# Kernel optimization log

Measured on AMD Instinct MI355X. Metric: run time of the kernel, lower is better.

The kernel has to match this reference:

```python
import jax, jax.numpy as jnp
import numpy as np

EMB = 1024
HEADS = 16
HEAD_DIM = EMB // HEADS
FF = 4 * EMB


def _gelu_tanh(x):
    c = jnp.sqrt(jnp.asarray(2.0 / jnp.pi, x.dtype))
    return 0.5 * x * (1.0 + jnp.tanh(c * (x + 0.044715 * x ** 3)))


def _layernorm(x, scale, shift, eps=1e-5):
    mean = jnp.mean(x, axis=-1, keepdims=True)
    var = jnp.mean((x - mean) ** 2, axis=-1, keepdims=True)
    return scale * (x - mean) / jnp.sqrt(var + eps) + shift


def setup_inputs() -> dict:
    key = jax.random.key(0)
    ks = jax.random.split(key, 8)
    s = 0.02
    return {
        "x": jax.random.normal(ks[0], (2, 2048, EMB), jnp.float32),
        "w_q": jax.random.normal(ks[1], (EMB, EMB), jnp.float32) * s,
        "w_k": jax.random.normal(ks[2], (EMB, EMB), jnp.float32) * s,
        "w_v": jax.random.normal(ks[3], (EMB, EMB), jnp.float32) * s,
        "w_o": jax.random.normal(ks[4], (EMB, EMB), jnp.float32) * s,
        "b_o": jnp.zeros((EMB,), jnp.float32),
        "ln1_scale": jnp.ones((EMB,), jnp.float32),
        "ln1_shift": jnp.zeros((EMB,), jnp.float32),
        "ln2_scale": jnp.ones((EMB,), jnp.float32),
        "ln2_shift": jnp.zeros((EMB,), jnp.float32),
        "w_ff1": jax.random.normal(ks[5], (EMB, FF), jnp.float32) * s,
        "b_ff1": jnp.zeros((FF,), jnp.float32),
        "w_ff2": jax.random.normal(ks[6], (FF, EMB), jnp.float32) * s,
        "b_ff2": jnp.zeros((EMB,), jnp.float32),
    }


def _attention(x, w_q, w_k, w_v, w_o, b_o):
    b, n, _ = x.shape
    q = (x @ w_q).reshape(b, n, HEADS, HEAD_DIM).transpose(0, 2, 1, 3)  # bhnd
    k = (x @ w_k).reshape(b, n, HEADS, HEAD_DIM).transpose(0, 2, 1, 3)
    v = (x @ w_v).reshape(b, n, HEADS, HEAD_DIM).transpose(0, 2, 1, 3)
    scores = jnp.einsum("bhqd,bhkd->bhqk", q, k)
    causal = jnp.triu(jnp.ones((n, n), bool), k=1)
    scores = jnp.where(causal, -jnp.inf, scores)
    # original scales AFTER masking (-inf stays -inf)
    attn = jax.nn.softmax(scores / jnp.sqrt(jnp.asarray(HEAD_DIM, x.dtype)), axis=-1)
    ctx = jnp.einsum("bhqk,bhkd->bhqd", attn, v)
    ctx = ctx.transpose(0, 2, 1, 3).reshape(b, n, EMB)
    return ctx @ w_o + b_o


def reference(x, w_q, w_k, w_v, w_o, b_o, ln1_scale, ln1_shift,
              ln2_scale, ln2_shift, w_ff1, b_ff1, w_ff2, b_ff2):
    h = _layernorm(x, ln1_scale, ln1_shift)
    h = _attention(h, w_q, w_k, w_v, w_o, b_o)
    x = x + h  # dropout is identity at drop_rate=0 / eval
    h = _layernorm(x, ln2_scale, ln2_shift)
    h = _gelu_tanh(h @ w_ff1 + b_ff1) @ w_ff2 + b_ff2
    return x + h
```

## Files before the change

### kernel.cpp

```cpp
#include <hip/hip_runtime.h>
#include <math.h>

#define EMB 1024
#define HEADS 16
#define HD 64
#define FF_DIM 4096
#define SEQ 2048
#define BATCH 2
#define NTOK (BATCH * SEQ)

typedef __bf16 bf16x8 __attribute__((ext_vector_type(8)));
typedef float f32x4 __attribute__((ext_vector_type(4)));

__device__ __forceinline__ unsigned short f2bf(float f) {
    union { float f; unsigned int u; } v; v.f = f;
    unsigned int r = v.u + 0x7fff + ((v.u >> 16) & 1);
    return (unsigned short)(r >> 16);
}

__device__ __forceinline__ unsigned int cvt_pk_bf16(float a, float b) {
    unsigned int r;
    asm("v_cvt_pk_bf16_f32 %0, %1, %2" : "=v"(r) : "v"(a), "v"(b));
    return r;
}

__device__ __forceinline__ float gelu_f(float x) {
    const float A = 1.5957691216057308f;
    const float B = 0.07135481282989427f;
    float zz = x * (A + B * x * x);
    return x * __builtin_amdgcn_rcpf(1.f + __expf(-zz));
}

#define GLOAD_LDS16(g, l)                                                      \
    __builtin_amdgcn_global_load_lds(                                          \
        (const __attribute__((address_space(1))) void*)(g),                    \
        (__attribute__((address_space(3))) void*)(l), 16, 0, 0)

__global__ __launch_bounds__(256) void ln_kernel(const float* __restrict__ x,
                                                 const float* __restrict__ scale,
                                                 const float* __restrict__ shift,
                                                 unsigned short* __restrict__ out) {
    int row = blockIdx.x;
    const float4* xr = (const float4*)(x + (size_t)row * EMB);
    int t = threadIdx.x;

    float4 v = xr[t];
    float s = v.x + v.y + v.z + v.w;
    float s2 = v.x * v.x + v.y * v.y + v.z * v.z + v.w * v.w;
    for (int o = 32; o > 0; o >>= 1) {
        s += __shfl_down(s, o, 64);
        s2 += __shfl_down(s2, o, 64);
    }
    __shared__ float red[4], red2[4];
    int wave = t >> 6;
    if ((t & 63) == 0) { red[wave] = s; red2[wave] = s2; }
    __syncthreads();
    if (t == 0) {
        float a = 0.f, b = 0.f;
#pragma unroll
        for (int i = 0; i < 4; i++) { a += red[i]; b += red2[i]; }
        red[0] = a; red2[0] = b;
    }
    __syncthreads();
    float mean = red[0] * (1.f / EMB);
    float var = red2[0] * (1.f / EMB) - mean * mean;
    float rstd = rsqrtf(var + 1e-5f);

    float4 sc = ((const float4*)scale)[t];
    float4 sh = ((const float4*)shift)[t];
    ushort4 o;
    o.x = f2bf(sc.x * (v.x - mean) * rstd + sh.x);
    o.y = f2bf(sc.y * (v.y - mean) * rstd + sh.y);
    o.z = f2bf(sc.z * (v.z - mean) * rstd + sh.z);
    o.w = f2bf(sc.w * (v.w - mean) * rstd + sh.w);
    ((ushort4*)(out + (size_t)row * EMB))[t] = o;
}

__global__ __launch_bounds__(256) void prep_kernel(
    const float* __restrict__ w0, const float* __restrict__ w1,
    const float* __restrict__ w2, const float* __restrict__ w3,
    const float* __restrict__ w4, const float* __restrict__ w5,
    unsigned short* __restrict__ o0, unsigned short* __restrict__ o1,
    unsigned short* __restrict__ o2, unsigned short* __restrict__ o3,
    unsigned short* __restrict__ o4, unsigned short* __restrict__ o5,
    const float* __restrict__ x, const float* __restrict__ ln1s,
    const float* __restrict__ ln1b, unsigned short* __restrict__ lnO) {
    __shared__ float tile[64][65];
    __shared__ float red[4], red2[4];
    int id = blockIdx.x;
    int t = threadIdx.x;

    if (id >= 3072) {
        int row = id - 3072;
        const float4* xr = (const float4*)(x + (size_t)row * EMB);
        float4 v = xr[t];
        float s = v.x + v.y + v.z + v.w;
        float s2 = v.x * v.x + v.y * v.y + v.z * v.z + v.w * v.w;
        for (int o = 32; o > 0; o >>= 1) {
            s += __shfl_down(s, o, 64);
            s2 += __shfl_down(s2, o, 64);
        }
        int wave = t >> 6;
        if ((t & 63) == 0) { red[wave] = s; red2[wave] = s2; }
        __syncthreads();
        if (t == 0) {
            float a = 0.f, b = 0.f;
#pragma unroll
            for (int i = 0; i < 4; i++) { a += red[i]; b += red2[i]; }
            red[0] = a; red2[0] = b;
        }
        __syncthreads();
        float mean = red[0] * (1.f / EMB);
        float var = red2[0] * (1.f / EMB) - mean * mean;
        float rstd = rsqrtf(var + 1e-5f);

        float4 sc = ((const float4*)ln1s)[t];
        float4 sh = ((const float4*)ln1b)[t];
        ushort4 o;
        o.x = f2bf(sc.x * (v.x - mean) * rstd + sh.x);
        o.y = f2bf(sc.y * (v.y - mean) * rstd + sh.y);
        o.z = f2bf(sc.z * (v.z - mean) * rstd + sh.z);
        o.w = f2bf(sc.w * (v.w - mean) * rstd + sh.w);
        ((ushort4*)(lnO + (size_t)row * EMB))[t] = o;
        return;
    }

    const float* src; unsigned short* dst; int K, N, lid;
    if (id < 256)       { src = w0; dst = o0; K = 1024; N = 1024; lid = id; }
    else if (id < 512)  { src = w1; dst = o1; K = 1024; N = 1024; lid = id - 256; }
    else if (id < 768)  { src = w2; dst = o2; K = 1024; N = 1024; lid = id - 512; }
    else if (id < 1024) { src = w3; dst = o3; K = 1024; N = 1024; lid = id - 768; }
    else if (id < 2048) { src = w4; dst = o4; K = 1024; N = 4096; lid = id - 1024; }
    else                { src = w5; dst = o5; K = 4096; N = 1024; lid = id - 2048; }
    int tn = N >> 6;
    int k0 = (lid / tn) << 6, n0 = (lid % tn) << 6;
    int rr = t >> 6, cc = t & 63;
#pragma unroll
    for (int i = 0; i < 16; i++) {
        int r = i * 4 + rr;
        tile[r][cc] = src[(size_t)(k0 + r) * N + n0 + cc];
    }
    __syncthreads();
#pragma unroll
    for (int i = 0; i < 16; i++) {
        int r = i * 4 + rr;
        dst[(size_t)(n0 + r) * K + k0 + cc] = f2bf(tile[cc][r]);
    }
}


__global__ __launch_bounds__(256) void ff1_gemm(
    const unsigned short* __restrict__ A,
    const unsigned short* __restrict__ Bt,
    unsigned short* __restrict__ C,
    const float* __restrict__ bias,
    int M, int N, int K) {
    __shared__ unsigned short As[2][128 * 64];
    __shared__ unsigned short Bs[2][128 * 64];

    const int t = threadIdx.x;
    const int w = t >> 6, lane = t & 63;
    const int m0 = blockIdx.x * 128, n0 = blockIdx.y * 128;

    const int srow = lane >> 3;
    const int sc = (lane & 7) ^ srow;
    const unsigned short* gA[4];
    const unsigned short* gB[4];
#pragma unroll
    for (int i = 0; i < 4; i++) {
        gA[i] = A + (size_t)(m0 + i * 32 + w * 8 + srow) * K + sc * 8;
        gB[i] = Bt + (size_t)(n0 + i * 32 + w * 8 + srow) * K + sc * 8;
    }

    const int mrow = (w >> 1) * 64, ncol = (w & 1) * 64;
    int ph[2];
#pragma unroll
    for (int s = 0; s < 2; s++) ph[s] = ((s * 4 + (lane >> 4)) ^ (lane & 7)) * 8;
    int abase[4], bbase[4];
#pragma unroll
    for (int i = 0; i < 4; i++) {
        abase[i] = (mrow + i * 16 + (lane & 15)) * 64;
        bbase[i] = (ncol + i * 16 + (lane & 15)) * 64;
    }

    f32x4 acc[4][4];
#pragma unroll
    for (int i = 0; i < 4; i++)
#pragma unroll
        for (int j = 0; j < 4; j++) acc[i][j] = (f32x4){0.f, 0.f, 0.f, 0.f};

#define STG1(b)                                                                \
    do {                                                                       \
        _Pragma("unroll") for (int i_ = 0; i_ < 4; i_++) {                     \
            GLOAD_LDS16(gA[i_], &As[b][(i_ * 32 + w * 8) * 64]);               \
            GLOAD_LDS16(gB[i_], &Bs[b][(i_ * 32 + w * 8) * 64]);               \
            gA[i_] += 64; gB[i_] += 64;                                        \
        }                                                                      \
    } while (0)

    STG1(0);
    const int nk = K >> 6;
    for (int it = 0; it < nk; it++) {
        const int buf = it & 1;
        __syncthreads();
        if (it + 1 < nk) STG1(buf ^ 1);
#pragma unroll
        for (int s = 0; s < 2; s++) {
            bf16x8 af[4], bfr[4];
#pragma unroll
            for (int i = 0; i < 4; i++) {
                af[i] = *reinterpret_cast<const bf16x8*>(&As[buf][abase[i] + ph[s]]);
                bfr[i] = *reinterpret_cast<const bf16x8*>(&Bs[buf][bbase[i] + ph[s]]);
            }
#pragma unroll
            for (int i = 0; i < 4; i++)
#pragma unroll
                for (int j = 0; j < 4; j++)
                    acc[i][j] = __builtin_amdgcn_mfma_f32_16x16x32_bf16(
                        af[i], bfr[j], acc[i][j], 0, 0, 0);
        }
    }
#undef STG1

    const int ccol = lane & 15;
    const int crow = (lane >> 4) << 2;
#pragma unroll
    for (int i = 0; i < 4; i++) {
#pragma unroll
        for (int j = 0; j < 4; j++) {
            int col = n0 + ncol + j * 16 + ccol;
            float badd = bias[col];
#pragma unroll
            for (int r = 0; r < 4; r++) {
                int row = m0 + mrow + i * 16 + crow + r;
                C[(size_t)row * N + col] = f2bf(gelu_f(acc[i][j][r] + badd));
            }
        }
    }
}

template <int EPI>
__global__ __launch_bounds__(256) void mfma_gemm_s64(
    const unsigned short* __restrict__ A,
    const unsigned short* __restrict__ Bt,
    float* __restrict__ C,
    const float* __restrict__ bias,
    const float* __restrict__ resid,
    int M, int N, int K) {
    __shared__ unsigned short As[2][64 * 64];
    __shared__ unsigned short Bs[2][64 * 64];

    const int t = threadIdx.x;
    const int w = t >> 6, lane = t & 63;
    const int m0 = blockIdx.x * 64, n0 = blockIdx.y * 64;

    const int srow = lane >> 3;
    const int sc = (lane & 7) ^ srow;
    const unsigned short* gA[2];
    const unsigned short* gB[2];
#pragma unroll
    for (int i = 0; i < 2; i++) {
        gA[i] = A + (size_t)(m0 + i * 32 + w * 8 + srow) * K + sc * 8;
        gB[i] = Bt + (size_t)(n0 + i * 32 + w * 8 + srow) * K + sc * 8;
    }

    int ph[2];
#pragma unroll
    for (int s = 0; s < 2; s++) ph[s] = ((s * 4 + (lane >> 4)) ^ (lane & 7)) * 8;
    const int mrow = (w >> 1) * 32, ncol = (w & 1) * 32;
    int abase[2], bbase[2];
#pragma unroll
    for (int i = 0; i < 2; i++) {
        abase[i] = (mrow + i * 16 + (lane & 15)) * 64;
        bbase[i] = (ncol + i * 16 + (lane & 15)) * 64;
    }

    f32x4 acc[2][2];
#pragma unroll
    for (int i = 0; i < 2; i++)
#pragma unroll
        for (int j = 0; j < 2; j++) acc[i][j] = (f32x4){0.f, 0.f, 0.f, 0.f};

#define STGS(b)                                                                \
    do {                                                                       \
        _Pragma("unroll") for (int i_ = 0; i_ < 2; i_++) {                     \
            GLOAD_LDS16(gA[i_], &As[b][(i_ * 32 + w * 8) * 64]);               \
            GLOAD_LDS16(gB[i_], &Bs[b][(i_ * 32 + w * 8) * 64]);               \
            gA[i_] += 64; gB[i_] += 64;                                        \
        }                                                                      \
    } while (0)

    STGS(0);
    const int nk = K >> 6;
    for (int it = 0; it < nk; it++) {
        const int buf = it & 1;
        __syncthreads();
        if (it + 1 < nk) STGS(buf ^ 1);
#pragma unroll
        for (int s = 0; s < 2; s++) {
            bf16x8 af[2], bfr[2];
#pragma unroll
            for (int i = 0; i < 2; i++) {
                af[i] = *reinterpret_cast<const bf16x8*>(&As[buf][abase[i] + ph[s]]);
                bfr[i] = *reinterpret_cast<const bf16x8*>(&Bs[buf][bbase[i] + ph[s]]);
            }
#pragma unroll
            for (int i = 0; i < 2; i++)
#pragma unroll
                for (int j = 0; j < 2; j++)
                    acc[i][j] = __builtin_amdgcn_mfma_f32_16x16x32_bf16(
                        af[i], bfr[j], acc[i][j], 0, 0, 0);
        }
    }
#undef STGS

    const int ccol = lane & 15;
    const int crow = (lane >> 4) << 2;
#pragma unroll
    for (int i = 0; i < 2; i++) {
#pragma unroll
        for (int j = 0; j < 2; j++) {
            int col = n0 + ncol + j * 16 + ccol;
            float badd = bias[col];
#pragma unroll
            for (int r = 0; r < 4; r++) {
                int row = m0 + mrow + i * 16 + crow + r;
                size_t idx = (size_t)row * N + col;
                if constexpr (EPI == 1) {
                    C[idx] = acc[i][j][r] + badd + resid[idx];
                } else {
                    C[idx] = C[idx] + acc[i][j][r] + badd;
                }
            }
        }
    }
}

__global__ __launch_bounds__(256) void qkv_gemm(
    const unsigned short* __restrict__ lnO,
    const unsigned short* __restrict__ wqkT,
    const unsigned short* __restrict__ wvT,
    unsigned short* __restrict__ q,
    unsigned short* __restrict__ kb,
    unsigned short* __restrict__ vT) {
    __shared__ unsigned short As[2][128 * 64];
    __shared__ unsigned short Bs[2][128 * 64];

    const int t = threadIdx.x;
    const int w = t >> 6, lane = t & 63;
    const int bid = blockIdx.x;
    const bool qk = bid < 512;

    const unsigned short *A, *Bt;
    int m0, n0, N;
    if (qk) {
        A = lnO; Bt = wqkT;
        m0 = (bid & 31) * 128; n0 = (bid >> 5) * 128; N = 2048;
    } else {
        int lb = bid - 512;
        A = wvT; Bt = lnO;
        m0 = (lb & 7) * 128; n0 = (lb >> 3) * 128; N = 4096;
    }
    const int K = 1024;

    const int srow = lane >> 3;
    const int sc = (lane & 7) ^ srow;
    const unsigned short* gA[4];
    const unsigned short* gB[4];
#pragma unroll
    for (int i = 0; i < 4; i++) {
        gA[i] = A + (size_t)(m0 + i * 32 + w * 8 + srow) * K + sc * 8;
        gB[i] = Bt + (size_t)(n0 + i * 32 + w * 8 + srow) * K + sc * 8;
    }

    const int mrow = (w >> 1) * 64, ncol = (w & 1) * 64;
    int ph[2];
#pragma unroll
    for (int s = 0; s < 2; s++) ph[s] = ((s * 4 + (lane >> 4)) ^ (lane & 7)) * 8;
    int abase[4], bbase[4];
#pragma unroll
    for (int i = 0; i < 4; i++) {
        abase[i] = (mrow + i * 16 + (lane & 15)) * 64;
        bbase[i] = (ncol + i * 16 + (lane & 15)) * 64;
    }

    f32x4 acc[4][4];
#pragma unroll
    for (int i = 0; i < 4; i++)
#pragma unroll
        for (int j = 0; j < 4; j++) acc[i][j] = (f32x4){0.f, 0.f, 0.f, 0.f};

#define STGQ(b)                                                                \
    do {                                                                       \
        _Pragma("unroll") for (int i_ = 0; i_ < 4; i_++) {                     \
            GLOAD_LDS16(gA[i_], &As[b][(i_ * 32 + w * 8) * 64]);               \
            GLOAD_LDS16(gB[i_], &Bs[b][(i_ * 32 + w * 8) * 64]);               \
            gA[i_] += 64; gB[i_] += 64;                                        \
        }                                                                      \
    } while (0)

    STGQ(0);
    const int nk = K >> 6;
    for (int it = 0; it < nk; it++) {
        const int buf = it & 1;
        __syncthreads();
        if (it + 1 < nk) STGQ(buf ^ 1);
#pragma unroll
        for (int s = 0; s < 2; s++) {
            bf16x8 af[4], bfr[4];
#pragma unroll
            for (int i = 0; i < 4; i++) {
                af[i] = *reinterpret_cast<const bf16x8*>(&As[buf][abase[i] + ph[s]]);
                bfr[i] = *reinterpret_cast<const bf16x8*>(&Bs[buf][bbase[i] + ph[s]]);
            }
#pragma unroll
            for (int i = 0; i < 4; i++)
#pragma unroll
                for (int j = 0; j < 4; j++)
                    acc[i][j] = __builtin_amdgcn_mfma_f32_16x16x32_bf16(
                        af[i], bfr[j], acc[i][j], 0, 0, 0);
        }
    }
#undef STGQ

    const int ccol = lane & 15;
    const int crow = (lane >> 4) << 2;
    unsigned short* dst;
    int nbase;
    if (qk) {
        dst = (n0 < 1024) ? q : kb;
        nbase = n0 & 1023;
    } else {
        dst = vT;
        nbase = n0;
    }
    const int ldc = qk ? 1024 : 4096;
#pragma unroll
    for (int i = 0; i < 4; i++) {
#pragma unroll
        for (int j = 0; j < 4; j++) {
            int col = nbase + ncol + j * 16 + ccol;
#pragma unroll
            for (int r = 0; r < 4; r++) {
                int row = m0 + mrow + i * 16 + crow + r;
                dst[(size_t)row * ldc + col] = f2bf(acc[i][j][r]);
            }
        }
    }
}

__global__ __launch_bounds__(256) void attn_mfma(
    const unsigned short* __restrict__ Q,
    const unsigned short* __restrict__ K,
    const unsigned short* __restrict__ Vt,
    unsigned short* __restrict__ O) {
    __shared__ unsigned short Ks[2][64 * 64];
    __shared__ unsigned short Vs[2][64 * 64];
    __shared__ unsigned short Ps[4][16 * 64];

    const int t = threadIdx.x;
    const int w = t >> 6, lane = t & 63;
    const int l15 = lane & 15, l4 = lane >> 4;
    const int bh = blockIdx.x;
    const int b = bh >> 4, h = bh & 15;
    const int pair = blockIdx.y;

    const int sr = (w << 3) + (lane >> 3);
    const int sc = lane & 7;
    const int c = sc ^ (sr & 7);
    const unsigned short* kbase = K + ((size_t)(b * SEQ)) * EMB + h * HD;
    const unsigned short* vbase = Vt + ((size_t)(h * HD)) * (size_t)NTOK + (size_t)b * SEQ;
    unsigned short* Pw = &Ps[w][0];

#define STAGE(k0s, buf)                                                        \
    do {                                                                       \
        GLOAD_LDS16(kbase + (size_t)((k0s) + sr) * EMB + c * 8,                \
                    &Ks[buf][(w << 3) * 64]);                                  \
        GLOAD_LDS16(kbase + (size_t)((k0s) + sr + 32) * EMB + c * 8,           \
                    &Ks[buf][((w << 3) + 32) * 64]);                           \
        GLOAD_LDS16(vbase + (size_t)sr * NTOK + (k0s) + c * 8,                 \
                    &Vs[buf][(w << 3) * 64]);                                  \
        GLOAD_LDS16(vbase + (size_t)(sr + 32) * NTOK + (k0s) + c * 8,          \
                    &Vs[buf][((w << 3) + 32) * 64]);                           \
    } while (0)

    const float C1 = 0.125f * 1.4426950408889634f;
    const float C2 = 3.0f * 1.4426950408889634f;

#pragma unroll
    for (int phase = 0; phase < 2; phase++) {
        const int qt = phase ? pair : (31 - pair);
        const int q0 = qt * 64;

        const unsigned short* qg =
            Q + ((size_t)(b * SEQ + q0 + w * 16 + l15)) * EMB + h * HD + l4 * 8;
        bf16x8 qf0 = *(const bf16x8*)qg;
        bf16x8 qf1 = *(const bf16x8*)(qg + 32);
        const int qrow = q0 + w * 16 + l15;

        float ls[4] = {0.f, 0.f, 0.f, 0.f};
        f32x4 Oacc[4];
#pragma unroll
        for (int j = 0; j < 4; j++) Oacc[j] = (f32x4){0.f, 0.f, 0.f, 0.f};

        const int ntiles = qt + 1;
        __syncthreads();
        STAGE(0, 0);
        for (int tile = 0; tile < ntiles; tile++) {
            const int k0 = tile * 64;
            const int buf = tile & 1;
            __syncthreads();
            if (tile + 1 < ntiles) STAGE(k0 + 64, buf ^ 1);

            f32x4 S[4];
#pragma unroll
            for (int j = 0; j < 4; j++) S[j] = (f32x4){0.f, 0.f, 0.f, 0.f};
            __builtin_amdgcn_s_setprio(1);
#pragma unroll
            for (int s = 0; s < 2; s++) {
                bf16x8 qf = s ? qf1 : qf0;
#pragma unroll
                for (int j = 0; j < 4; j++) {
                    int rk = 16 * j + l15;
                    int phys = (s * 4 + l4) ^ (rk & 7);
                    bf16x8 kf = *(const bf16x8*)&Ks[buf][rk * 64 + phys * 8];
                    S[j] = __builtin_amdgcn_mfma_f32_16x16x32_bf16(kf, qf, S[j], 0, 0, 0);
                }
            }
            __builtin_amdgcn_s_setprio(0);

            if (tile == ntiles - 1) {
#pragma unroll
                for (int j = 0; j < 4; j++)
#pragma unroll
                    for (int r = 0; r < 4; r++) {
                        float e = exp2f(S[j][r] * C1 - C2);
                        if (k0 + 16 * j + 4 * l4 + r > qrow) e = 0.f;
                        S[j][r] = e;
                    }
            } else {
#pragma unroll
                for (int j = 0; j < 4; j++)
#pragma unroll
                    for (int r = 0; r < 4; r++)
                        S[j][r] = exp2f(S[j][r] * C1 - C2);
            }

#pragma unroll
            for (int j = 0; j < 4; j++) {
                ls[j] += S[j][0] + S[j][1] + S[j][2] + S[j][3];
                unsigned int lo = cvt_pk_bf16(S[j][0], S[j][1]);
                unsigned int hi = cvt_pk_bf16(S[j][2], S[j][3]);
                int chunk = (2 * j + (l4 >> 1)) ^ (l15 & 7);
                uint2 val; val.x = lo; val.y = hi;
                *reinterpret_cast<uint2*>(&Pw[l15 * 64 + chunk * 8 + (l4 & 1) * 4]) = val;
            }

            __builtin_amdgcn_s_setprio(1);
#pragma unroll
            for (int s = 0; s < 2; s++) {
                int pch = (4 * s + l4) ^ (l15 & 7);
                bf16x8 pf = *(const bf16x8*)&Pw[l15 * 64 + pch * 8];
#pragma unroll
                for (int j = 0; j < 4; j++) {
                    int rv = 16 * j + l15;
                    int vph = (s * 4 + l4) ^ (rv & 7);
                    bf16x8 vf = *(const bf16x8*)&Vs[buf][rv * 64 + vph * 8];
                    Oacc[j] = __builtin_amdgcn_mfma_f32_16x16x32_bf16(vf, pf, Oacc[j], 0, 0, 0);
                }
            }
            __builtin_amdgcn_s_setprio(0);
        }

        float l = ls[0] + ls[1] + ls[2] + ls[3];
        l += __shfl_xor(l, 16, 64);
        l += __shfl_xor(l, 32, 64);
        float inv = 1.f / l;
        size_t rowb = (size_t)(b * SEQ + qrow) * EMB + h * HD;
#pragma unroll
        for (int j = 0; j < 4; j++) {
            unsigned int lo = cvt_pk_bf16(Oacc[j][0] * inv, Oacc[j][1] * inv);
            unsigned int hi = cvt_pk_bf16(Oacc[j][2] * inv, Oacc[j][3] * inv);
            uint2 val; val.x = lo; val.y = hi;
            *reinterpret_cast<uint2*>(&O[rowb + 16 * j + 4 * l4]) = val;
        }
    }
#undef STAGE
}

extern "C" void kernel_launch(void* const* d_in, const int* in_sizes, int n_in,
                              void* d_out, int out_size, void* d_ws, size_t ws_size,
                              hipStream_t stream) {
    const float* x     = (const float*)d_in[0];
    const float* w_q   = (const float*)d_in[1];
    const float* w_k   = (const float*)d_in[2];
    const float* w_v   = (const float*)d_in[3];
    const float* w_o   = (const float*)d_in[4];
    const float* b_o   = (const float*)d_in[5];
    const float* ln1s  = (const float*)d_in[6];
    const float* ln1b  = (const float*)d_in[7];
    const float* ln2s  = (const float*)d_in[8];
    const float* ln2b  = (const float*)d_in[9];
    const float* w_ff1 = (const float*)d_in[10];
    const float* b_ff1 = (const float*)d_in[11];
    const float* w_ff2 = (const float*)d_in[12];
    const float* b_ff2 = (const float*)d_in[13];
    float* out = (float*)d_out;

    char* p = (char*)d_ws;
    unsigned short* lnO  = (unsigned short*)p; p += (size_t)NTOK * EMB * 2;
    unsigned short* q    = (unsigned short*)p; p += (size_t)NTOK * EMB * 2;
    unsigned short* kbuf = (unsigned short*)p; p += (size_t)NTOK * EMB * 2;
    unsigned short* vT   = (unsigned short*)p; p += (size_t)NTOK * EMB * 2;
    unsigned short* ctx  = (unsigned short*)p; p += (size_t)NTOK * EMB * 2;
    unsigned short* ff1a = (unsigned short*)p; p += (size_t)NTOK * FF_DIM * 2;
    unsigned short* wqkT = (unsigned short*)p; p += (size_t)2 * EMB * EMB * 2;
    unsigned short* wvT  = (unsigned short*)p; p += (size_t)EMB * EMB * 2;
    unsigned short* woT  = (unsigned short*)p; p += (size_t)EMB * EMB * 2;
    unsigned short* wf1T = (unsigned short*)p; p += (size_t)FF_DIM * EMB * 2;
    unsigned short* wf2T = (unsigned short*)p; p += (size_t)EMB * FF_DIM * 2;

    dim3 blk(256);
    dim3 gS64(NTOK / 64, EMB / 64);
    dim3 gFF1(NTOK / 128, FF_DIM / 128);
    dim3 gAttn(BATCH * HEADS, 16);

    prep_kernel<<<3072 + NTOK, blk, 0, stream>>>(
        w_q, w_k, w_v, w_o, w_ff1, w_ff2,
        wqkT, wqkT + (size_t)EMB * EMB, wvT, woT, wf1T, wf2T,
        x, ln1s, ln1b, lnO);
    qkv_gemm<<<768, blk, 0, stream>>>(lnO, wqkT, wvT, q, kbuf, vT);
    attn_mfma<<<gAttn, blk, 0, stream>>>(q, kbuf, vT, ctx);
    mfma_gemm_s64<1><<<gS64, blk, 0, stream>>>(ctx, woT, out, b_o, x, NTOK, EMB, EMB);
    ln_kernel<<<NTOK, blk, 0, stream>>>(out, ln2s, ln2b, ctx);
    ff1_gemm<<<gFF1, blk, 0, stream>>>(ctx, wf1T, ff1a, b_ff1, NTOK, FF_DIM, EMB);
    mfma_gemm_s64<3><<<gS64, blk, 0, stream>>>(ff1a, wf2T, out, b_ff2, nullptr, NTOK, EMB, FF_DIM);
}
```

Before: 327.3 us.

## Split-K the FF2 GEMM with atomic accumulation and prefetch residual in out-proj

The FF2 GEMM (K=4096) is replaced by a split-K kernel. The K dimension is halved across twice as many blocks (2048 instead of 1024), and partial results go into the output with float atomics, with the bias added only by the first half. The aim is more parallelism and occupancy for the long-K GEMM, paid for with atomic read-modify-write traffic and an order of accumulation that is no longer fixed. Separately, the out-projection epilogue now loads its residual values before the main loop, so their latency is hidden behind the MFMA work at the cost of more registers.

```diff
diff --git a/kernel.cpp b/kernel.cpp
--- a/kernel.cpp
+++ b/kernel.cpp
@@ -275,6 +275,23 @@
         bbase[i] = (ncol + i * 16 + (lane & 15)) * 64;
     }
 
+    const int ccol = lane & 15;
+    const int crow = (lane >> 4) << 2;
+
+    float rpre[2][2][4];
+    if constexpr (EPI == 1) {
+#pragma unroll
+        for (int i = 0; i < 2; i++)
+#pragma unroll
+            for (int j = 0; j < 2; j++)
+#pragma unroll
+                for (int r = 0; r < 4; r++) {
+                    int row = m0 + mrow + i * 16 + crow + r;
+                    int col = n0 + ncol + j * 16 + ccol;
+                    rpre[i][j][r] = resid[(size_t)row * N + col];
+                }
+    }
+
     f32x4 acc[2][2];
 #pragma unroll
     for (int i = 0; i < 2; i++)
@@ -314,8 +331,6 @@
     }
 #undef STGS
 
-    const int ccol = lane & 15;
-    const int crow = (lane >> 4) << 2;
 #pragma unroll
     for (int i = 0; i < 2; i++) {
 #pragma unroll
@@ -327,10 +342,106 @@
                 int row = m0 + mrow + i * 16 + crow + r;
                 size_t idx = (size_t)row * N + col;
                 if constexpr (EPI == 1) {
-                    C[idx] = acc[i][j][r] + badd + resid[idx];
+                    C[idx] = acc[i][j][r] + badd + rpre[i][j][r];
                 } else {
                     C[idx] = C[idx] + acc[i][j][r] + badd;
                 }
+            }
+        }
+    }
+}
+
+__global__ __launch_bounds__(256) void ff2_s64(
+    const unsigned short* __restrict__ A,
+    const unsigned short* __restrict__ Bt,
+    float* __restrict__ C,
+    const float* __restrict__ bias,
+    int M, int N, int K) {
+    __shared__ unsigned short As[2][64 * 64];
+    __shared__ unsigned short Bs[2][64 * 64];
+
+    const int t = threadIdx.x;
+    const int w = t >> 6, lane = t & 63;
+    const int id = blockIdx.x;
+    const int n0 = (id & 15) * 64;
+    const int ks = (id >> 4) & 1;
+    const int m0 = (id >> 5) * 64;
+    const int khalf = K >> 1;
+    const int kbeg = ks * khalf;
+
+    const int srow = lane >> 3;
+    const int sc = (lane & 7) ^ srow;
+    const unsigned short* gA[2];
+    const unsigned short* gB[2];
+#pragma unroll
+    for (int i = 0; i < 2; i++) {
+        gA[i] = A + (size_t)(m0 + i * 32 + w * 8 + srow) * K + kbeg + sc * 8;
+        gB[i] = Bt + (size_t)(n0 + i * 32 + w * 8 + srow) * K + kbeg + sc * 8;
+    }
+
+    int ph[2];
+#pragma unroll
+    for (int s = 0; s < 2; s++) ph[s] = ((s * 4 + (lane >> 4)) ^ (lane & 7)) * 8;
+    const int mrow = (w >> 1) * 32, ncol = (w & 1) * 32;
+    int abase[2], bbase[2];
+#pragma unroll
+    for (int i = 0; i < 2; i++) {
+        abase[i] = (mrow + i * 16 + (lane & 15)) * 64;
+        bbase[i] = (ncol + i * 16 + (lane & 15)) * 64;
+    }
+
+    f32x4 acc[2][2];
+#pragma unroll
+    for (int i = 0; i < 2; i++)
+#pragma unroll
+        for (int j = 0; j < 2; j++) acc[i][j] = (f32x4){0.f, 0.f, 0.f, 0.f};
+
+#define STGF(b)                                                                \
+    do {                                                                       \
+        _Pragma("unroll") for (int i_ = 0; i_ < 2; i_++) {                     \
+            GLOAD_LDS16(gA[i_], &As[b][(i_ * 32 + w * 8) * 64]);               \
+            GLOAD_LDS16(gB[i_], &Bs[b][(i_ * 32 + w * 8) * 64]);               \
+            gA[i_] += 64; gB[i_] += 64;                                        \
+        }                                                                      \
+    } while (0)
+
+    STGF(0);
+    const int nk = khalf >> 6;
+    for (int it = 0; it < nk; it++) {
+        const int buf = it & 1;
+        __syncthreads();
+        if (it + 1 < nk) STGF(buf ^ 1);
+#pragma unroll
+        for (int s = 0; s < 2; s++) {
+            bf16x8 af[2], bfr[2];
+#pragma unroll
+            for (int i = 0; i < 2; i++) {
+                af[i] = *reinterpret_cast<const bf16x8*>(&As[buf][abase[i] + ph[s]]);
+                bfr[i] = *reinterpret_cast<const bf16x8*>(&Bs[buf][bbase[i] + ph[s]]);
+            }
+#pragma unroll
+            for (int i = 0; i < 2; i++)
+#pragma unroll
+                for (int j = 0; j < 2; j++)
+                    acc[i][j] = __builtin_amdgcn_mfma_f32_16x16x32_bf16(
+                        af[i], bfr[j], acc[i][j], 0, 0, 0);
+        }
+    }
+#undef STGF
+
+    const int ccol = lane & 15;
+    const int crow = (lane >> 4) << 2;
+#pragma unroll
+    for (int i = 0; i < 2; i++) {
+#pragma unroll
+        for (int j = 0; j < 2; j++) {
+            int col = n0 + ncol + j * 16 + ccol;
+            float badd = ks == 0 ? bias[col] : 0.f;
+#pragma unroll
+            for (int r = 0; r < 4; r++) {
+                int row = m0 + mrow + i * 16 + crow + r;
+                size_t idx = (size_t)row * N + col;
+                unsafeAtomicAdd(&C[idx], acc[i][j][r] + badd);
             }
         }
     }
@@ -634,5 +745,5 @@
     mfma_gemm_s64<1><<<gS64, blk, 0, stream>>>(ctx, woT, out, b_o, x, NTOK, EMB, EMB);
     ln_kernel<<<NTOK, blk, 0, stream>>>(out, ln2s, ln2b, ctx);
     ff1_gemm<<<gFF1, blk, 0, stream>>>(ctx, wf1T, ff1a, b_ff1, NTOK, FF_DIM, EMB);
-    mfma_gemm_s64<3><<<gS64, blk, 0, stream>>>(ff1a, wf2T, out, b_ff2, nullptr, NTOK, EMB, FF_DIM);
-}
+    ff2_s64<<<2048, blk, 0, stream>>>(ff1a, wf2T, out, b_ff2, NTOK, EMB, FF_DIM);
+}
```

New measurement: 340.4 us. +4.0%, slower.
